# Optimization experiments

Hardware: AMD Instinct MI355X
Metric: run time of the kernel (lower is better)

Reference implementation:

```python
import jax, jax.numpy as jnp
import numpy as np

H = 32          # heads
E = 32          # head dim = mdl_channels // heads (must equal heads per module bug)
C = 1024        # mdl_channels == in_channels
MAXP = 128      # max_position_embeddings
EPS = 1e-5


def _layernorm(x, g, b):
    mu = jnp.mean(x, axis=-1, keepdims=True)
    var = jnp.var(x, axis=-1, keepdims=True)
    return (x - mu) * jax.lax.rsqrt(var + EPS) * g + b


def setup_inputs() -> dict:
    key = jax.random.key(0)
    ks = jax.random.split(key, 16)
    s = 0.02
    N, L = 4, 1024
    inp = {
        "x": jax.random.normal(ks[0], (N, L, C), jnp.float32),
        "Wq": jax.random.normal(ks[1], (C, C), jnp.float32) * s,
        "bq": jnp.zeros((C,), jnp.float32),
        "Wk": jax.random.normal(ks[2], (C, C), jnp.float32) * s,
        "bk": jnp.zeros((C,), jnp.float32),
        "Wv": jax.random.normal(ks[3], (C, C), jnp.float32) * s,
        "bv": jnp.zeros((C,), jnp.float32),
        "dist_emb": jax.random.normal(ks[4], (2 * MAXP + 1, E), jnp.float32) * s,
        "ln1_g": jnp.ones((C,), jnp.float32),
        "ln1_b": jnp.zeros((C,), jnp.float32),
        "ln2_g": jnp.ones((C,), jnp.float32),
        "ln2_b": jnp.zeros((C,), jnp.float32),
        "W1": jax.random.normal(ks[5], (C, C), jnp.float32) * s,
        "b1": jnp.zeros((C,), jnp.float32),
        "W2": jax.random.normal(ks[6], (C, C), jnp.float32) * s,
        "b2": jnp.zeros((C,), jnp.float32),
    }
    return inp


def reference(x, Wq, bq, Wk, bk, Wv, bv, dist_emb, ln1_g, ln1_b,
              ln2_g, ln2_b, W1, b1, W2, b2):
    N, L, _ = x.shape
    # QKV projections -> (N, L, H, E)
    q = (x @ Wq + bq).reshape(N, L, H, E)
    k = (x @ Wk + bk).reshape(N, L, H, E)
    v = (x @ Wv + bv).reshape(N, L, H, E)

    temp = 1.0 / np.sqrt(E).astype(np.float32)
    # content scores (N, H, L, S)
    QK = jnp.einsum('nlhe,nshe->nhls', q, k)
    # relative position scores (disentangled attention)
    pos = jnp.arange(L)
    dist = jnp.clip(pos[:, None] - pos[None, :], -MAXP, MAXP) + MAXP  # (L, L)
    pe = dist_emb[dist]                                              # (L, L, E)
    QK = QK + jnp.einsum('nlhe,lse->nhls', q, pe) \
            + jnp.einsum('nshe,lse->nhls', k, pe)
    A = jax.nn.softmax(temp * QK, axis=-1)          # dropout: eval mode (identity)
    t = jnp.einsum('nhls,nshe->nlhe', A, v).reshape(N, L, C)

    h = _layernorm(t + x, ln1_g, ln1_b)             # AddNorm (attention)
    m = jax.nn.relu(h @ W1 + b1) @ W2 + b2          # 2-layer MLP
    out = _layernorm(m + h, ln2_g, ln2_b)           # AddNorm (mlp)
    return jnp.swapaxes(out, 0, 1)                  # 'n f c -> f n c'
```

## Files before the change

kernel.cpp:

```cpp
#include <hip/hip_runtime.h>

#define H_ 32
#define E_ 32
#define C_ 1024
#define L_ 1024
#define N_ 4
#define M_ 4096
#define NH_ 128
#define D_ 257
#define DPAD 272
#define QDP 264
#define TEMP_ 0.17677669529663687f
#define QSCALE_ (TEMP_ * 1.4426950408889634f)

typedef unsigned short u16;
typedef __attribute__((ext_vector_type(8))) short short8;
typedef __attribute__((ext_vector_type(4))) float f32x4;
typedef __attribute__((ext_vector_type(4))) unsigned short u16x4;

__device__ __forceinline__ u16 f2bf(float f) {
  union { float f; unsigned u; } v; v.f = f;
  unsigned r = v.u + 0x7fffu + ((v.u >> 16) & 1u);
  return (u16)(r >> 16);
}
__device__ __forceinline__ float bf2f(u16 h) {
  union { unsigned u; float f; } v; v.u = ((unsigned)h) << 16;
  return v.f;
}
__device__ __forceinline__ f32x4 mfma16(short8 a, short8 b, f32x4 c) {
  return __builtin_amdgcn_mfma_f32_16x16x32_bf16(a, b, c, 0, 0, 0);
}
__device__ __forceinline__ float ex2(float x) {
#if __has_builtin(__builtin_amdgcn_exp2f)
  return __builtin_amdgcn_exp2f(x);
#else
  float r;
  asm("v_exp_f32 %0, %1\n\ts_nop 1" : "=v"(r) : "v"(x));
  return r;
#endif
}
__device__ __forceinline__ void gld16(const u16* g, u16* l) {
  __builtin_amdgcn_global_load_lds(
      (const __attribute__((address_space(1))) unsigned int*)g,
      (__attribute__((address_space(3))) unsigned int*)l, 16, 0, 0);
}

__global__ __launch_bounds__(256) void misc_kernel(
    const float* __restrict__ x, const float* __restrict__ demb,
    const float* __restrict__ bq, const float* __restrict__ bk,
    const float* __restrict__ bv, u16* __restrict__ xb,
    u16* __restrict__ demb_b, float* __restrict__ bqkv) {
  const int b = blockIdx.x, tid = threadIdx.x;
  if (b < 4096) {
    int i = b * 256 + tid;
    f32x4 v = reinterpret_cast<const f32x4*>(x)[i];
    u16x4 o2;
    o2[0] = f2bf(v[0]); o2[1] = f2bf(v[1]); o2[2] = f2bf(v[2]); o2[3] = f2bf(v[3]);
    reinterpret_cast<u16x4*>(xb)[i] = o2;
  } else {
    int i = (b - 4096) * 256 + tid;
    if (i < DPAD * E_) demb_b[i] = (i < D_ * E_) ? f2bf(demb[i]) : (u16)0;
    if (i < C_) { bqkv[i] = bq[i]; bqkv[C_ + i] = bk[i]; bqkv[2 * C_ + i] = bv[i]; }
  }
}

__global__ __launch_bounds__(256) void transpose_w_kernel(
    const float* __restrict__ Wq, const float* __restrict__ Wk,
    const float* __restrict__ Wv, const float* __restrict__ W1,
    const float* __restrict__ W2, u16* __restrict__ out_base) {
  __shared__ float tile[32][33];
  const int z = blockIdx.z;
  const float* in = (z == 0) ? Wq : (z == 1) ? Wk : (z == 2) ? Wv : (z == 3) ? W1 : W2;
  u16* out = out_base + (size_t)z * C_ * C_;
  int j0 = blockIdx.x * 32, c0 = blockIdx.y * 32;
#pragma unroll
  for (int i = 0; i < 4; ++i) {
    int cy = threadIdx.y + i * 8;
    tile[cy][threadIdx.x] = in[(size_t)(c0 + cy) * C_ + j0 + threadIdx.x];
  }
  __syncthreads();
#pragma unroll
  for (int i = 0; i < 4; ++i) {
    int jy = threadIdx.y + i * 8;
    out[(size_t)(j0 + jy) * C_ + c0 + threadIdx.x] = f2bf(tile[threadIdx.x][jy]);
  }
}

template <int EPI>
__global__ __launch_bounds__(256) void gemm128_kernel(
    const u16* __restrict__ A, const u16* __restrict__ Bt, int K,
    const float* __restrict__ bias,
    u16* __restrict__ out0, u16* __restrict__ out1, u16* __restrict__ out2) {
  __shared__ u16 As[128 * 64];
  __shared__ u16 Bs[128 * 64];
  const int bid = blockIdx.x;
  const int m0 = (bid & 31) << 7;
  const int n0 = (bid >> 5) << 7;
  const int tid = threadIdx.x;
  const int w = tid >> 6, lane = tid & 63, lhi = lane >> 4, llo = lane & 15;
  const int wr = w >> 1, wc = w & 1;
  const int w4 = w << 2;
  const int srow = lane >> 3, scol = (lane & 7) << 3;
  f32x4 acc[4][4] = {};
  for (int k0 = 0; k0 < K; k0 += 64) {
#pragma unroll
    for (int j = 0; j < 4; ++j) {
      const int seg = w4 + j;
      const int row = (seg << 3) + srow;
      gld16(&A[(size_t)(m0 + row) * K + k0 + scol], &As[seg << 9]);
      gld16(&Bt[(size_t)(n0 + row) * K + k0 + scol], &Bs[seg << 9]);
    }
    __syncthreads();
#pragma unroll
    for (int kk = 0; kk < 2; ++kk) {
      const int ko = (kk << 5) + lhi * 8;
      short8 af[4], bf[4];
#pragma unroll
      for (int mi = 0; mi < 4; ++mi)
        af[mi] = *reinterpret_cast<const short8*>(&As[(wr * 64 + mi * 16 + llo) * 64 + ko]);
#pragma unroll
      for (int ni = 0; ni < 4; ++ni)
        bf[ni] = *reinterpret_cast<const short8*>(&Bs[(wc * 64 + ni * 16 + llo) * 64 + ko]);
#pragma unroll
      for (int mi = 0; mi < 4; ++mi)
#pragma unroll
        for (int ni = 0; ni < 4; ++ni)
          acc[mi][ni] = mfma16(af[mi], bf[ni], acc[mi][ni]);
    }
    __syncthreads();
  }
#pragma unroll
  for (int mi = 0; mi < 4; ++mi)
#pragma unroll
    for (int ni = 0; ni < 4; ++ni)
#pragma unroll
      for (int r = 0; r < 4; ++r) {
        int row = m0 + wr * 64 + mi * 16 + lhi * 4 + r;
        int col = n0 + wc * 64 + ni * 16 + llo;
        float v = acc[mi][ni][r] + bias[col];
        if constexpr (EPI == 0) {
          int which = col >> 10, jj = col & 1023, h = jj >> 5, e2 = jj & 31;
          int n = row >> 10, l = row & 1023;
          int nh = (n << 5) | h;
          if (which == 0) v *= QSCALE_;
          u16 bvv = f2bf(v);
          if (which == 0)      out0[((size_t)((nh << 10) | l)) * 32 + e2] = bvv;
          else if (which == 1) out1[((size_t)((nh << 10) | l)) * 32 + e2] = bvv;
          else                 out2[(((size_t)(nh * 32 + e2)) << 10) | l] = bvv;
        } else if constexpr (EPI == 1) {
          out0[(size_t)row * C_ + col] = f2bf(fmaxf(v, 0.f));
        } else {
          out0[(size_t)row * C_ + col] = f2bf(v);
        }
      }
}

__global__ __launch_bounds__(256) void qdkd_kernel(
    const u16* __restrict__ src, const u16* __restrict__ demb,
    u16* __restrict__ dst, u16* __restrict__ aux0, u16* __restrict__ aux256) {
  const int wt = blockIdx.x * 4 + (threadIdx.x >> 6);
  const int lane = threadIdx.x & 63, lhi = lane >> 4, llo = lane & 15;
  const int m0 = wt << 4;
  short8 a = *reinterpret_cast<const short8*>(&src[(size_t)(m0 + llo) * E_ + lhi * 8]);
#pragma unroll
  for (int ct = 0; ct < 17; ++ct) {
    int d = ct * 16 + llo;
    short8 b = {0, 0, 0, 0, 0, 0, 0, 0};
    if (d < D_) b = *reinterpret_cast<const short8*>(&demb[d * E_ + lhi * 8]);
    f32x4 c = {};
    c = mfma16(a, b, c);
    if (d < D_) {
#pragma unroll
      for (int r = 0; r < 4; ++r) {
        u16 val = f2bf(c[r] * QSCALE_);
        dst[(size_t)(m0 + lhi * 4 + r) * D_ + d] = val;
        if (d == 0)   aux0[m0 + lhi * 4 + r] = val;
        if (d == 256) aux256[m0 + lhi * 4 + r] = val;
      }
    }
  }
}

__global__ __launch_bounds__(256, 4) void attn_kernel(
    const u16* __restrict__ qw, const u16* __restrict__ kw,
    const u16* __restrict__ vT, const u16* __restrict__ dembp,
    const u16* __restrict__ KDg, const u16* __restrict__ kd0a,
    const u16* __restrict__ kd256a, u16* __restrict__ tb) {
  __shared__ u16 QDs[64 * QDP];
  __shared__ u16 Pbuf[4 * 512];
  const int bid = blockIdx.x;
  const int nh = bid & (NH_ - 1);
  const int l0 = (bid >> 7) << 6;
  const int tid = threadIdx.x;
  const int w = tid >> 6, lane = tid & 63, lhi = lane >> 4, llo = lane & 15;
  const int lw0 = l0 + (w << 4);
  const int lg = lw0 + llo;
  const int lrow = (w << 4) + llo;

  const u16* qb  = qw + (size_t)nh * (L_ * E_);
  const u16* kb  = kw + (size_t)nh * (L_ * E_);
  const u16* vb  = vT + (size_t)nh * (E_ * L_);
  const u16* kdg = KDg + (size_t)nh * ((size_t)L_ * D_);
  const u16* k0g = kd0a + (size_t)nh * L_;
  const u16* k2g = kd256a + (size_t)nh * L_;

  const short8 qA = *(const short8*)&qb[(size_t)lg * E_ + lhi * 8];
  const int qr4 = (w << 4) + (lhi << 2);

#pragma unroll
  for (int dt = 0; dt < 16; ++dt) {
    short8 db = *(const short8*)&dembp[(dt * 16 + llo) * E_ + lhi * 8];
    f32x4 qd = {};
    qd = mfma16(qA, db, qd);
#pragma unroll
    for (int r = 0; r < 4; ++r)
      QDs[(qr4 + r) * QDP + dt * 16 + llo] = f2bf(qd[r]);
  }
  {
    short8 db = *(const short8*)&dembp[(size_t)(256 + llo) * E_ + lhi * 8];
    f32x4 qd = {};
    qd = mfma16(qA, db, qd);
    if (llo == 0) {
#pragma unroll
      for (int r = 0; r < 4; ++r)
        QDs[(qr4 + r) * QDP + 256] = f2bf(qd[r]);
    }
  }

  const float qd0   = bf2f(QDs[lrow * QDP + 0]);
  const float qd256 = bf2f(QDs[lrow * QDP + 256]);

  f32x4 o0 = {}, o1 = {};
  float lacc = 0.f;
  char* Pw = reinterpret_cast<char*>(&Pbuf[w * 512]);

  for (int s0 = 0; s0 < L_; s0 += 32) {
    short8 kA0 = *(const short8*)&kb[(size_t)(s0 + llo) * E_ + lhi * 8];
    short8 kA1 = *(const short8*)&kb[(size_t)(s0 + 16 + llo) * E_ + lhi * 8];
    f32x4 st0 = {}, st1 = {};
    st0 = mfma16(kA0, qA, st0);
    st1 = mfma16(kA1, qA, st1);

    float p[8];
    const bool far_hi = (lw0 - (s0 + 31)) >= 128;
    const bool far_lo = (s0 - (lw0 + 15)) >= 128;
    if (far_hi || far_lo) {
      const float qdc = far_hi ? qd256 : qd0;
      const u16* kcg = far_hi ? k2g : k0g;
      u16x4 kc0 = *(const u16x4*)&kcg[s0 + lhi * 4];
      u16x4 kc1 = *(const u16x4*)&kcg[s0 + 16 + lhi * 4];
#pragma unroll
      for (int r = 0; r < 4; ++r) {
        p[r]     = ex2(st0[r] + qdc + bf2f(kc0[r]));
        p[4 + r] = ex2(st1[r] + qdc + bf2f(kc1[r]));
      }
    } else {
#pragma unroll
      for (int i = 0; i < 2; ++i)
#pragma unroll
        for (int r = 0; r < 4; ++r) {
          const int scol = s0 + i * 16 + lhi * 4 + r;
          int d = lg - scol;
          d = (d < -128 ? -128 : (d > 128 ? 128 : d)) + 128;
          float qd = bf2f(QDs[lrow * QDP + d]);
          float kd = bf2f(kdg[(size_t)scol * D_ + d]);
          p[i * 4 + r] = ex2((i ? st1[r] : st0[r]) + qd + kd);
        }
    }
    lacc += ((p[0] + p[1]) + (p[2] + p[3])) + ((p[4] + p[5]) + (p[6] + p[7]));

#pragma unroll
    for (int i = 0; i < 2; ++i)
#pragma unroll
      for (int b = 0; b < 2; ++b) {
        union { float f; unsigned u; } a0, a1;
        a0.f = p[i * 4 + 2 * b]; a1.f = p[i * 4 + 2 * b + 1];
        unsigned wv = ((a0.u + 0x8000u) >> 16) | ((a1.u + 0x8000u) & 0xffff0000u);
        int u = (i * 4 + lhi) ^ (llo & 6);
        *reinterpret_cast<unsigned*>(Pw + llo * 64 + u * 8 + b * 4) = wv;
      }
    short8 pB = *reinterpret_cast<const short8*>(
        Pw + llo * 64 + (((lhi * 2) ^ (llo & 6)) * 8));
    short8 vA0 = *(const short8*)&vb[(size_t)llo * L_ + s0 + lhi * 8];
    short8 vA1 = *(const short8*)&vb[(size_t)(16 + llo) * L_ + s0 + lhi * 8];
    o0 = mfma16(vA0, pB, o0);
    o1 = mfma16(vA1, pB, o1);
  }

  float l2 = lacc + __shfl_xor(lacc, 16);
  float lt = l2 + __shfl_xor(l2, 32);
  const float inv = 1.0f / lt;

  const int n = nh >> 5, h = nh & 31;
  const size_t obase = (((size_t)((n << 10) | lg)) * 32 + h) * 32;
  u16x4 w0, w1;
#pragma unroll
  for (int r = 0; r < 4; ++r) {
    w0[r] = f2bf(o0[r] * inv);
    w1[r] = f2bf(o1[r] * inv);
  }
  *reinterpret_cast<u16x4*>(&tb[obase + lhi * 4]) = w0;
  *reinterpret_cast<u16x4*>(&tb[obase + 16 + lhi * 4]) = w1;
}

__global__ __launch_bounds__(256) void ln1_kernel(
    const u16* __restrict__ tbuf, const float* __restrict__ x,
    const float* __restrict__ g, const float* __restrict__ b,
    u16* __restrict__ hb) {
  __shared__ float red[8];
  const int row = blockIdx.x, tid = threadIdx.x;
  const size_t base = (size_t)row * C_ + tid * 4;
  f32x4 xv = *reinterpret_cast<const f32x4*>(&x[base]);
  u16x4 tv = *reinterpret_cast<const u16x4*>(&tbuf[base]);
  float v[4]; float s1 = 0.f, s2 = 0.f;
#pragma unroll
  for (int i = 0; i < 4; ++i) {
    v[i] = xv[i] + bf2f(tv[i]);
    s1 += v[i]; s2 += v[i] * v[i];
  }
#pragma unroll
  for (int off = 32; off >= 1; off >>= 1) {
    s1 += __shfl_xor(s1, off); s2 += __shfl_xor(s2, off);
  }
  if ((tid & 63) == 0) { red[tid >> 6] = s1; red[4 + (tid >> 6)] = s2; }
  __syncthreads();
  float S1 = red[0] + red[1] + red[2] + red[3];
  float S2 = red[4] + red[5] + red[6] + red[7];
  float mu = S1 * (1.f / C_);
  float rs = rsqrtf(S2 * (1.f / C_) - mu * mu + 1e-5f);
#pragma unroll
  for (int i = 0; i < 4; ++i) {
    int c = tid * 4 + i;
    hb[base + i] = f2bf((v[i] - mu) * rs * g[c] + b[c]);
  }
}

__global__ __launch_bounds__(256) void ln2_kernel(
    const u16* __restrict__ mb, const u16* __restrict__ hb,
    const float* __restrict__ g, const float* __restrict__ b,
    float* __restrict__ out) {
  __shared__ float red[8];
  const int row = blockIdx.x, tid = threadIdx.x;
  const size_t base = (size_t)row * C_ + tid * 4;
  u16x4 mv = *reinterpret_cast<const u16x4*>(&mb[base]);
  u16x4 hv = *reinterpret_cast<const u16x4*>(&hb[base]);
  float v[4]; float s1 = 0.f, s2 = 0.f;
#pragma unroll
  for (int i = 0; i < 4; ++i) {
    v[i] = bf2f(mv[i]) + bf2f(hv[i]);
    s1 += v[i]; s2 += v[i] * v[i];
  }
#pragma unroll
  for (int off = 32; off >= 1; off >>= 1) {
    s1 += __shfl_xor(s1, off); s2 += __shfl_xor(s2, off);
  }
  if ((tid & 63) == 0) { red[tid >> 6] = s1; red[4 + (tid >> 6)] = s2; }
  __syncthreads();
  float S1 = red[0] + red[1] + red[2] + red[3];
  float S2 = red[4] + red[5] + red[6] + red[7];
  float mu = S1 * (1.f / C_);
  float rs = rsqrtf(S2 * (1.f / C_) - mu * mu + 1e-5f);
  const int n = row >> 10, l = row & 1023;
  const size_t ob = (size_t)(l * N_ + n) * C_ + tid * 4;
#pragma unroll
  for (int i = 0; i < 4; ++i) {
    int c = tid * 4 + i;
    out[ob + i] = (v[i] - mu) * rs * g[c] + b[c];
  }
}

extern "C" void kernel_launch(void* const* d_in, const int* in_sizes, int n_in,
                              void* d_out, int out_size, void* d_ws, size_t ws_size,
                              hipStream_t stream) {
  const float* x    = (const float*)d_in[0];
  const float* Wq   = (const float*)d_in[1];
  const float* bq   = (const float*)d_in[2];
  const float* Wk   = (const float*)d_in[3];
  const float* bk   = (const float*)d_in[4];
  const float* Wv   = (const float*)d_in[5];
  const float* bv   = (const float*)d_in[6];
  const float* demb = (const float*)d_in[7];
  const float* g1   = (const float*)d_in[8];
  const float* b1ln = (const float*)d_in[9];
  const float* g2   = (const float*)d_in[10];
  const float* b2ln = (const float*)d_in[11];
  const float* W1   = (const float*)d_in[12];
  const float* b1   = (const float*)d_in[13];
  const float* W2   = (const float*)d_in[14];
  const float* b2   = (const float*)d_in[15];
  float* outp = (float*)d_out;

  size_t o = 0;
  auto alloc = [&](size_t bytes) { size_t r = o; o += (bytes + 255) & ~(size_t)255; return r; };
  const size_t xb_o    = alloc((size_t)M_ * C_ * 2);
  const size_t wqkv_o  = alloc((size_t)3 * C_ * C_ * 2);
  const size_t w1_o    = alloc((size_t)C_ * C_ * 2);
  const size_t w2_o    = alloc((size_t)C_ * C_ * 2);
  const size_t bqkv_o  = alloc((size_t)3 * C_ * 4);
  const size_t demb_o  = alloc((size_t)DPAD * E_ * 2);
  const size_t q_o     = alloc((size_t)NH_ * L_ * E_ * 2);
  const size_t k_o     = alloc((size_t)NH_ * L_ * E_ * 2);
  const size_t vt_o    = alloc((size_t)NH_ * L_ * E_ * 2);
  const size_t kd_o    = alloc((size_t)NH_ * L_ * D_ * 2);
  const size_t kd0_o   = alloc((size_t)NH_ * L_ * 2);
  const size_t kd256_o = alloc((size_t)NH_ * L_ * 2);
  const size_t t_o     = alloc((size_t)M_ * C_ * 2);
  const size_t h_o     = alloc((size_t)M_ * C_ * 2);
  const size_t m1_o    = alloc((size_t)M_ * C_ * 2);
  const size_t m_o     = alloc((size_t)M_ * C_ * 2);
  if (o > ws_size) return;

  char* ws = (char*)d_ws;
  u16*   xb     = (u16*)(ws + xb_o);
  u16*   wqkv_t = (u16*)(ws + wqkv_o);
  u16*   w1_t   = (u16*)(ws + w1_o);
  u16*   w2_t   = (u16*)(ws + w2_o);
  float* bqkv   = (float*)(ws + bqkv_o);
  u16*   demb_b = (u16*)(ws + demb_o);
  u16*   q_ws   = (u16*)(ws + q_o);
  u16*   k_ws   = (u16*)(ws + k_o);
  u16*   vT_ws  = (u16*)(ws + vt_o);
  u16*   KD     = (u16*)(ws + kd_o);
  u16*   kd0a   = (u16*)(ws + kd0_o);
  u16*   kd256a = (u16*)(ws + kd256_o);
  u16*   t_b16  = (u16*)(ws + t_o);
  u16*   h_b16  = (u16*)(ws + h_o);
  u16*   m1_b16 = (u16*)(ws + m1_o);
  u16*   m_b16  = (u16*)(ws + m_o);

  misc_kernel<<<4096 + 34, 256, 0, stream>>>(x, demb, bq, bk, bv, xb, demb_b, bqkv);
  dim3 tb_(32, 8), tg_(32, 32, 5);
  transpose_w_kernel<<<tg_, tb_, 0, stream>>>(Wq, Wk, Wv, W1, W2, wqkv_t);

  gemm128_kernel<0><<<32 * 24, 256, 0, stream>>>(xb, wqkv_t, C_, bqkv, q_ws, k_ws, vT_ws);

  qdkd_kernel<<<2048, 256, 0, stream>>>(k_ws, demb_b, KD, kd0a, kd256a);

  attn_kernel<<<NH_ * 16, 256, 0, stream>>>(q_ws, k_ws, vT_ws, demb_b, KD, kd0a, kd256a, t_b16);

  ln1_kernel<<<M_, 256, 0, stream>>>(t_b16, x, g1, b1ln, h_b16);

  gemm128_kernel<1><<<32 * 8, 256, 0, stream>>>(h_b16, w1_t, C_, b1, m1_b16, nullptr, nullptr);
  gemm128_kernel<2><<<32 * 8, 256, 0, stream>>>(m1_b16, w2_t, C_, b2, m_b16, nullptr, nullptr);

  ln2_kernel<<<M_, 256, 0, stream>>>(m_b16, h_b16, g2, b2ln, outp);
}
```

Baseline: 270.0 us.

## Software-pipeline P·V MFMA across iterations with double-buffered P tile in LDS

Double-buffers the per-wave P tile in LDS so each iteration's P·V MFMA runs one step behind the score computation, overlapping its LDS read and V loads with the next QK MFMA and exp work. V loads move to the top of the iteration. The QD row stride is shrunk from 264 to 256, and the d=256 column is stashed in a register through a small LDS scratch, which keeps total LDS about the same. This adds a branch in the near-diagonal path and changes the LDS bank mapping of QD rows, which may create bank conflicts.

After: 269.5 us. Within noise of the previous version (-0.2%).

```diff
diff --git a/kernel.cpp b/kernel.cpp
--- a/kernel.cpp
+++ b/kernel.cpp
@@ -9,7 +9,7 @@
 #define NH_ 128
 #define D_ 257
 #define DPAD 272
-#define QDP 264
+#define QDS 256
 #define TEMP_ 0.17677669529663687f
 #define QSCALE_ (TEMP_ * 1.4426950408889634f)
 
@@ -186,8 +186,8 @@
     const u16* __restrict__ vT, const u16* __restrict__ dembp,
     const u16* __restrict__ KDg, const u16* __restrict__ kd0a,
     const u16* __restrict__ kd256a, u16* __restrict__ tb) {
-  __shared__ u16 QDs[64 * QDP];
-  __shared__ u16 Pbuf[4 * 512];
+  __shared__ u16 QDs[64 * QDS];
+  __shared__ u16 Pbuf[4 * 1024];
   const int bid = blockIdx.x;
   const int nh = bid & (NH_ - 1);
   const int l0 = (bid >> 7) << 6;
@@ -207,6 +207,8 @@
   const short8 qA = *(const short8*)&qb[(size_t)lg * E_ + lhi * 8];
   const int qr4 = (w << 4) + (lhi << 2);
 
+  char* Pw = reinterpret_cast<char*>(&Pbuf[w * 1024]);
+
 #pragma unroll
   for (int dt = 0; dt < 16; ++dt) {
     short8 db = *(const short8*)&dembp[(dt * 16 + llo) * E_ + lhi * 8];
@@ -214,32 +216,42 @@
     qd = mfma16(qA, db, qd);
 #pragma unroll
     for (int r = 0; r < 4; ++r)
-      QDs[(qr4 + r) * QDP + dt * 16 + llo] = f2bf(qd[r]);
-  }
+      QDs[(qr4 + r) * QDS + dt * 16 + llo] = f2bf(qd[r]);
+  }
+  float qd256;
   {
     short8 db = *(const short8*)&dembp[(size_t)(256 + llo) * E_ + lhi * 8];
     f32x4 qd = {};
     qd = mfma16(qA, db, qd);
+    u16* stash = reinterpret_cast<u16*>(Pw);
     if (llo == 0) {
 #pragma unroll
-      for (int r = 0; r < 4; ++r)
-        QDs[(qr4 + r) * QDP + 256] = f2bf(qd[r]);
-    }
-  }
-
-  const float qd0   = bf2f(QDs[lrow * QDP + 0]);
-  const float qd256 = bf2f(QDs[lrow * QDP + 256]);
+      for (int r = 0; r < 4; ++r) stash[(lhi << 2) + r] = f2bf(qd[r]);
+    }
+    qd256 = bf2f(stash[llo]);
+  }
+  const float qd0 = bf2f(QDs[lrow * QDS + 0]);
 
   f32x4 o0 = {}, o1 = {};
   float lacc = 0.f;
-  char* Pw = reinterpret_cast<char*>(&Pbuf[w * 512]);
+  short8 vp0, vp1;
 
   for (int s0 = 0; s0 < L_; s0 += 32) {
+    const int buf = (s0 >> 5) & 1;
     short8 kA0 = *(const short8*)&kb[(size_t)(s0 + llo) * E_ + lhi * 8];
     short8 kA1 = *(const short8*)&kb[(size_t)(s0 + 16 + llo) * E_ + lhi * 8];
+    short8 vc0 = *(const short8*)&vb[(size_t)llo * L_ + s0 + lhi * 8];
+    short8 vc1 = *(const short8*)&vb[(size_t)(16 + llo) * L_ + s0 + lhi * 8];
     f32x4 st0 = {}, st1 = {};
     st0 = mfma16(kA0, qA, st0);
     st1 = mfma16(kA1, qA, st1);
+
+    if (s0) {
+      short8 pB = *reinterpret_cast<const short8*>(
+          Pw + (buf ^ 1) * 1024 + llo * 64 + (((lhi * 2) ^ (llo & 6)) * 8));
+      o0 = mfma16(vp0, pB, o0);
+      o1 = mfma16(vp1, pB, o1);
+    }
 
     float p[8];
     const bool far_hi = (lw0 - (s0 + 31)) >= 128;
@@ -262,7 +274,8 @@
           const int scol = s0 + i * 16 + lhi * 4 + r;
           int d = lg - scol;
           d = (d < -128 ? -128 : (d > 128 ? 128 : d)) + 128;
-          float qd = bf2f(QDs[lrow * QDP + d]);
+          int dc = d > 255 ? 255 : d;
+          float qd = (d == 256) ? qd256 : bf2f(QDs[lrow * QDS + dc]);
           float kd = bf2f(kdg[(size_t)scol * D_ + d]);
           p[i * 4 + r] = ex2((i ? st1[r] : st0[r]) + qd + kd);
         }
@@ -277,14 +290,16 @@
         a0.f = p[i * 4 + 2 * b]; a1.f = p[i * 4 + 2 * b + 1];
         unsigned wv = ((a0.u + 0x8000u) >> 16) | ((a1.u + 0x8000u) & 0xffff0000u);
         int u = (i * 4 + lhi) ^ (llo & 6);
-        *reinterpret_cast<unsigned*>(Pw + llo * 64 + u * 8 + b * 4) = wv;
+        *reinterpret_cast<unsigned*>(Pw + buf * 1024 + llo * 64 + u * 8 + b * 4) = wv;
       }
+    vp0 = vc0; vp1 = vc1;
+  }
+
+  {
     short8 pB = *reinterpret_cast<const short8*>(
-        Pw + llo * 64 + (((lhi * 2) ^ (llo & 6)) * 8));
-    short8 vA0 = *(const short8*)&vb[(size_t)llo * L_ + s0 + lhi * 8];
-    short8 vA1 = *(const short8*)&vb[(size_t)(16 + llo) * L_ + s0 + lhi * 8];
-    o0 = mfma16(vA0, pB, o0);
-    o1 = mfma16(vA1, pB, o1);
+        Pw + 1024 + llo * 64 + (((lhi * 2) ^ (llo & 6)) * 8));
+    o0 = mfma16(vp0, pB, o0);
+    o1 = mfma16(vp1, pB, o1);
   }
 
   float l2 = lacc + __shfl_xor(lacc, 16);
```

## Store key-distance scores in diagonal band layout and reverse query-distance table

Applied to the files above, without the earlier changes.

The K·dist_emb table is rewritten into a band layout indexed by query row, so that in the attention kernel each lane reads contiguous 4-element vectors instead of strided scalar gathers with per-element clamping. The query-distance shared table is stored reversed with a 257 stride so interior tiles also load contiguous vectors. A three-way split separates far tiles, fully interior tiles (vector loads) and boundary tiles (select between band and clamped endpoint values). This adds branching and relies on correct band index arithmetic. The 257 stride may also introduce misaligned vector reads from shared memory.

Result: slower. 324.1 us (+20.0%).

```diff
diff --git a/kernel.cpp b/kernel.cpp
--- a/kernel.cpp
+++ b/kernel.cpp
@@ -9,7 +9,6 @@
 #define NH_ 128
 #define D_ 257
 #define DPAD 272
-#define QDP 264
 #define TEMP_ 0.17677669529663687f
 #define QSCALE_ (TEMP_ * 1.4426950408889634f)
 
@@ -156,26 +155,30 @@
 }
 
 __global__ __launch_bounds__(256) void qdkd_kernel(
-    const u16* __restrict__ src, const u16* __restrict__ demb,
-    u16* __restrict__ dst, u16* __restrict__ aux0, u16* __restrict__ aux256) {
+    const u16* __restrict__ src, const u16* __restrict__ dembp,
+    u16* __restrict__ kdb, u16* __restrict__ aux0, u16* __restrict__ aux256) {
   const int wt = blockIdx.x * 4 + (threadIdx.x >> 6);
   const int lane = threadIdx.x & 63, lhi = lane >> 4, llo = lane & 15;
   const int m0 = wt << 4;
+  const int head = m0 >> 10;
+  u16* kdbh = kdb + (size_t)head * ((size_t)L_ * D_);
   short8 a = *reinterpret_cast<const short8*>(&src[(size_t)(m0 + llo) * E_ + lhi * 8]);
 #pragma unroll
   for (int ct = 0; ct < 17; ++ct) {
     int d = ct * 16 + llo;
-    short8 b = {0, 0, 0, 0, 0, 0, 0, 0};
-    if (d < D_) b = *reinterpret_cast<const short8*>(&demb[d * E_ + lhi * 8]);
+    short8 b = *reinterpret_cast<const short8*>(&dembp[d * E_ + lhi * 8]);
     f32x4 c = {};
     c = mfma16(a, b, c);
     if (d < D_) {
 #pragma unroll
       for (int r = 0; r < 4; ++r) {
         u16 val = f2bf(c[r] * QSCALE_);
-        dst[(size_t)(m0 + lhi * 4 + r) * D_ + d] = val;
-        if (d == 0)   aux0[m0 + lhi * 4 + r] = val;
-        if (d == 256) aux256[m0 + lhi * 4 + r] = val;
+        const int mrow = m0 + (lhi << 2) + r;
+        const int sl = mrow & 1023;
+        const int lp = sl + d - 128;
+        if (lp >= 0 && lp < L_) kdbh[256 * lp + sl + 128] = val;
+        if (d == 0)   aux0[mrow] = val;
+        if (d == 256) aux256[mrow] = val;
       }
     }
   }
@@ -184,9 +187,9 @@
 __global__ __launch_bounds__(256, 4) void attn_kernel(
     const u16* __restrict__ qw, const u16* __restrict__ kw,
     const u16* __restrict__ vT, const u16* __restrict__ dembp,
-    const u16* __restrict__ KDg, const u16* __restrict__ kd0a,
+    const u16* __restrict__ kdb, const u16* __restrict__ kd0a,
     const u16* __restrict__ kd256a, u16* __restrict__ tb) {
-  __shared__ u16 QDs[64 * QDP];
+  __shared__ u16 QDs[64 * 257];
   __shared__ u16 Pbuf[4 * 512];
   const int bid = blockIdx.x;
   const int nh = bid & (NH_ - 1);
@@ -200,7 +203,7 @@
   const u16* qb  = qw + (size_t)nh * (L_ * E_);
   const u16* kb  = kw + (size_t)nh * (L_ * E_);
   const u16* vb  = vT + (size_t)nh * (E_ * L_);
-  const u16* kdg = KDg + (size_t)nh * ((size_t)L_ * D_);
+  const u16* kdl = kdb + (size_t)nh * ((size_t)L_ * D_) + 256 * (size_t)lg + 128;
   const u16* k0g = kd0a + (size_t)nh * L_;
   const u16* k2g = kd256a + (size_t)nh * L_;
 
@@ -214,7 +217,7 @@
     qd = mfma16(qA, db, qd);
 #pragma unroll
     for (int r = 0; r < 4; ++r)
-      QDs[(qr4 + r) * QDP + dt * 16 + llo] = f2bf(qd[r]);
+      QDs[(qr4 + r) * 257 + 256 - (dt * 16 + llo)] = f2bf(qd[r]);
   }
   {
     short8 db = *(const short8*)&dembp[(size_t)(256 + llo) * E_ + lhi * 8];
@@ -222,13 +225,13 @@
     qd = mfma16(qA, db, qd);
     if (llo == 0) {
 #pragma unroll
-      for (int r = 0; r < 4; ++r)
-        QDs[(qr4 + r) * QDP + 256] = f2bf(qd[r]);
+      for (int r = 0; r < 4; ++r) QDs[(qr4 + r) * 257 + 0] = f2bf(qd[r]);
     }
   }
-
-  const float qd0   = bf2f(QDs[lrow * QDP + 0]);
-  const float qd256 = bf2f(QDs[lrow * QDP + 256]);
+  const int qrb = lrow * 257;
+  const int qpb = qrb + 128 - lg;
+  const float qd_d0   = bf2f(QDs[qrb + 256]);
+  const float qd_d256 = bf2f(QDs[qrb + 0]);
 
   f32x4 o0 = {}, o1 = {};
   float lacc = 0.f;
@@ -242,11 +245,11 @@
     st1 = mfma16(kA1, qA, st1);
 
     float p[8];
-    const bool far_hi = (lw0 - (s0 + 31)) >= 128;
-    const bool far_lo = (s0 - (lw0 + 15)) >= 128;
-    if (far_hi || far_lo) {
-      const float qdc = far_hi ? qd256 : qd0;
-      const u16* kcg = far_hi ? k2g : k0g;
+    const int delta = lw0 - s0;
+    if (delta >= 159 || delta <= -143) {
+      const bool fh = delta >= 159;
+      const float qdc = fh ? qd_d256 : qd_d0;
+      const u16* kcg = fh ? k2g : k0g;
       u16x4 kc0 = *(const u16x4*)&kcg[s0 + lhi * 4];
       u16x4 kc1 = *(const u16x4*)&kcg[s0 + 16 + lhi * 4];
 #pragma unroll
@@ -254,17 +257,36 @@
         p[r]     = ex2(st0[r] + qdc + bf2f(kc0[r]));
         p[4 + r] = ex2(st1[r] + qdc + bf2f(kc1[r]));
       }
+    } else if (delta <= 112 && delta >= -97) {
+      u16x4 qv0 = *(const u16x4*)&QDs[qpb + s0 + (lhi << 2)];
+      u16x4 qv1 = *(const u16x4*)&QDs[qpb + s0 + 16 + (lhi << 2)];
+      u16x4 kv0 = *(const u16x4*)&kdl[s0 + (lhi << 2)];
+      u16x4 kv1 = *(const u16x4*)&kdl[s0 + 16 + (lhi << 2)];
+#pragma unroll
+      for (int r = 0; r < 4; ++r) {
+        p[r]     = ex2(st0[r] + bf2f(qv0[r]) + bf2f(kv0[r]));
+        p[4 + r] = ex2(st1[r] + bf2f(qv1[r]) + bf2f(kv1[r]));
+      }
     } else {
+      u16x4 kv0 = *(const u16x4*)&kdl[s0 + (lhi << 2)];
+      u16x4 kv1 = *(const u16x4*)&kdl[s0 + 16 + (lhi << 2)];
+      u16x4 a00 = *(const u16x4*)&k0g[s0 + (lhi << 2)];
+      u16x4 a01 = *(const u16x4*)&k0g[s0 + 16 + (lhi << 2)];
+      u16x4 a20 = *(const u16x4*)&k2g[s0 + (lhi << 2)];
+      u16x4 a21 = *(const u16x4*)&k2g[s0 + 16 + (lhi << 2)];
 #pragma unroll
       for (int i = 0; i < 2; ++i)
 #pragma unroll
         for (int r = 0; r < 4; ++r) {
-          const int scol = s0 + i * 16 + lhi * 4 + r;
-          int d = lg - scol;
-          d = (d < -128 ? -128 : (d > 128 ? 128 : d)) + 128;
-          float qd = bf2f(QDs[lrow * QDP + d]);
-          float kd = bf2f(kdg[(size_t)scol * D_ + d]);
-          p[i * 4 + r] = ex2((i ? st1[r] : st0[r]) + qd + kd);
+          const int scol = s0 + i * 16 + (lhi << 2) + r;
+          int j = scol - lg + 128;
+          int jc = j < 0 ? 0 : (j > 256 ? 256 : j);
+          float qd = bf2f(QDs[qrb + jc]);
+          u16 kin = i ? kv1[r] : kv0[r];
+          u16 klo = i ? a01[r] : a00[r];
+          u16 khi = i ? a21[r] : a20[r];
+          u16 ksel = (j <= 0) ? khi : ((j >= 256) ? klo : kin);
+          p[i * 4 + r] = ex2((i ? st1[r] : st0[r]) + qd + bf2f(ksel));
         }
     }
     lacc += ((p[0] + p[1]) + (p[2] + p[3])) + ((p[4] + p[5]) + (p[6] + p[7]));
@@ -401,7 +423,7 @@
   const size_t q_o     = alloc((size_t)NH_ * L_ * E_ * 2);
   const size_t k_o     = alloc((size_t)NH_ * L_ * E_ * 2);
   const size_t vt_o    = alloc((size_t)NH_ * L_ * E_ * 2);
-  const size_t kd_o    = alloc((size_t)NH_ * L_ * D_ * 2);
+  const size_t kdb_o   = alloc((size_t)NH_ * L_ * D_ * 2);
   const size_t kd0_o   = alloc((size_t)NH_ * L_ * 2);
   const size_t kd256_o = alloc((size_t)NH_ * L_ * 2);
   const size_t t_o     = alloc((size_t)M_ * C_ * 2);
@@ -420,7 +442,7 @@
   u16*   q_ws   = (u16*)(ws + q_o);
   u16*   k_ws   = (u16*)(ws + k_o);
   u16*   vT_ws  = (u16*)(ws + vt_o);
-  u16*   KD     = (u16*)(ws + kd_o);
+  u16*   kdb    = (u16*)(ws + kdb_o);
   u16*   kd0a   = (u16*)(ws + kd0_o);
   u16*   kd256a = (u16*)(ws + kd256_o);
   u16*   t_b16  = (u16*)(ws + t_o);
@@ -434,9 +456,9 @@
 
   gemm128_kernel<0><<<32 * 24, 256, 0, stream>>>(xb, wqkv_t, C_, bqkv, q_ws, k_ws, vT_ws);
 
-  qdkd_kernel<<<2048, 256, 0, stream>>>(k_ws, demb_b, KD, kd0a, kd256a);
-
-  attn_kernel<<<NH_ * 16, 256, 0, stream>>>(q_ws, k_ws, vT_ws, demb_b, KD, kd0a, kd256a, t_b16);
+  qdkd_kernel<<<2048, 256, 0, stream>>>(k_ws, demb_b, kdb, kd0a, kd256a);
+
+  attn_kernel<<<NH_ * 16, 256, 0, stream>>>(q_ws, k_ws, vT_ws, demb_b, kdb, kd0a, kd256a, t_b16);
 
   ln1_kernel<<<M_, 256, 0, stream>>>(t_b16, x, g1, b1ln, h_b16);
 
```

## Add 64x128 GEMM for MLP layers and shrink attention QD shared buffer

Applied to the files above, without the earlier changes.

Adds a gemm64 kernel with 64-row tiles so the two MLP GEMMs launch 512 blocks instead of 256, aiming to fill more of the GPU's compute units. In the attention kernel the per-row QD table stride drops from 264 to 256. The d==256 entry is now passed through a register via a small stash in the P buffer, which cuts LDS use and may raise occupancy. The qdkd kernel also drops a bounds check on the demb load, so it relies on the padded demb buffer; the new 256-element stride could bring back LDS bank conflicts.

After: 264.7 us. No clear change (-1.9%).

```diff
diff --git a/kernel.cpp b/kernel.cpp
--- a/kernel.cpp
+++ b/kernel.cpp
@@ -9,7 +9,7 @@
 #define NH_ 128
 #define D_ 257
 #define DPAD 272
-#define QDP 264
+#define QDS 256
 #define TEMP_ 0.17677669529663687f
 #define QSCALE_ (TEMP_ * 1.4426950408889634f)
 
@@ -155,6 +155,66 @@
       }
 }
 
+template <int EPI>
+__global__ __launch_bounds__(256, 4) void gemm64_kernel(
+    const u16* __restrict__ A, const u16* __restrict__ Bt, int K,
+    const float* __restrict__ bias, u16* __restrict__ out0) {
+  __shared__ u16 As[64 * 64];
+  __shared__ u16 Bs[128 * 64];
+  const int bid = blockIdx.x;
+  const int m0 = (bid & 63) << 6;
+  const int n0 = (bid >> 6) << 7;
+  const int tid = threadIdx.x;
+  const int w = tid >> 6, lane = tid & 63, lhi = lane >> 4, llo = lane & 15;
+  const int wr = w >> 1, wc = w & 1;
+  const int srow = lane >> 3, scol = (lane & 7) << 3;
+  f32x4 acc[2][4] = {};
+  for (int k0 = 0; k0 < K; k0 += 64) {
+#pragma unroll
+    for (int j = 0; j < 2; ++j) {
+      const int seg = w * 2 + j;
+      const int row = (seg << 3) + srow;
+      gld16(&A[(size_t)(m0 + row) * K + k0 + scol], &As[seg << 9]);
+    }
+#pragma unroll
+    for (int j = 0; j < 4; ++j) {
+      const int seg = w * 4 + j;
+      const int row = (seg << 3) + srow;
+      gld16(&Bt[(size_t)(n0 + row) * K + k0 + scol], &Bs[seg << 9]);
+    }
+    __syncthreads();
+#pragma unroll
+    for (int kk = 0; kk < 2; ++kk) {
+      const int ko = (kk << 5) + lhi * 8;
+      short8 af[2], bf[4];
+#pragma unroll
+      for (int mi = 0; mi < 2; ++mi)
+        af[mi] = *reinterpret_cast<const short8*>(&As[(wr * 32 + mi * 16 + llo) * 64 + ko]);
+#pragma unroll
+      for (int ni = 0; ni < 4; ++ni)
+        bf[ni] = *reinterpret_cast<const short8*>(&Bs[(wc * 64 + ni * 16 + llo) * 64 + ko]);
+#pragma unroll
+      for (int mi = 0; mi < 2; ++mi)
+#pragma unroll
+        for (int ni = 0; ni < 4; ++ni)
+          acc[mi][ni] = mfma16(af[mi], bf[ni], acc[mi][ni]);
+    }
+    __syncthreads();
+  }
+#pragma unroll
+  for (int mi = 0; mi < 2; ++mi)
+#pragma unroll
+    for (int ni = 0; ni < 4; ++ni)
+#pragma unroll
+      for (int r = 0; r < 4; ++r) {
+        int row = m0 + wr * 32 + mi * 16 + lhi * 4 + r;
+        int col = n0 + wc * 64 + ni * 16 + llo;
+        float v = acc[mi][ni][r] + bias[col];
+        if constexpr (EPI == 1) out0[(size_t)row * C_ + col] = f2bf(fmaxf(v, 0.f));
+        else                    out0[(size_t)row * C_ + col] = f2bf(v);
+      }
+}
+
 __global__ __launch_bounds__(256) void qdkd_kernel(
     const u16* __restrict__ src, const u16* __restrict__ demb,
     u16* __restrict__ dst, u16* __restrict__ aux0, u16* __restrict__ aux256) {
@@ -165,8 +225,7 @@
 #pragma unroll
   for (int ct = 0; ct < 17; ++ct) {
     int d = ct * 16 + llo;
-    short8 b = {0, 0, 0, 0, 0, 0, 0, 0};
-    if (d < D_) b = *reinterpret_cast<const short8*>(&demb[d * E_ + lhi * 8]);
+    short8 b = *reinterpret_cast<const short8*>(&demb[d * E_ + lhi * 8]);
     f32x4 c = {};
     c = mfma16(a, b, c);
     if (d < D_) {
@@ -186,7 +245,7 @@
     const u16* __restrict__ vT, const u16* __restrict__ dembp,
     const u16* __restrict__ KDg, const u16* __restrict__ kd0a,
     const u16* __restrict__ kd256a, u16* __restrict__ tb) {
-  __shared__ u16 QDs[64 * QDP];
+  __shared__ u16 QDs[64 * QDS];
   __shared__ u16 Pbuf[4 * 512];
   const int bid = blockIdx.x;
   const int nh = bid & (NH_ - 1);
@@ -207,6 +266,8 @@
   const short8 qA = *(const short8*)&qb[(size_t)lg * E_ + lhi * 8];
   const int qr4 = (w << 4) + (lhi << 2);
 
+  char* Pw = reinterpret_cast<char*>(&Pbuf[w * 512]);
+
 #pragma unroll
   for (int dt = 0; dt < 16; ++dt) {
     short8 db = *(const short8*)&dembp[(dt * 16 + llo) * E_ + lhi * 8];
@@ -214,25 +275,24 @@
     qd = mfma16(qA, db, qd);
 #pragma unroll
     for (int r = 0; r < 4; ++r)
-      QDs[(qr4 + r) * QDP + dt * 16 + llo] = f2bf(qd[r]);
-  }
+      QDs[(qr4 + r) * QDS + dt * 16 + llo] = f2bf(qd[r]);
+  }
+  float qd256;
   {
     short8 db = *(const short8*)&dembp[(size_t)(256 + llo) * E_ + lhi * 8];
     f32x4 qd = {};
     qd = mfma16(qA, db, qd);
+    u16* stash = reinterpret_cast<u16*>(Pw);
     if (llo == 0) {
 #pragma unroll
-      for (int r = 0; r < 4; ++r)
-        QDs[(qr4 + r) * QDP + 256] = f2bf(qd[r]);
-    }
-  }
-
-  const float qd0   = bf2f(QDs[lrow * QDP + 0]);
-  const float qd256 = bf2f(QDs[lrow * QDP + 256]);
+      for (int r = 0; r < 4; ++r) stash[(lhi << 2) + r] = f2bf(qd[r]);
+    }
+    qd256 = bf2f(stash[llo]);
+  }
+  const float qd0 = bf2f(QDs[lrow * QDS + 0]);
 
   f32x4 o0 = {}, o1 = {};
   float lacc = 0.f;
-  char* Pw = reinterpret_cast<char*>(&Pbuf[w * 512]);
 
   for (int s0 = 0; s0 < L_; s0 += 32) {
     short8 kA0 = *(const short8*)&kb[(size_t)(s0 + llo) * E_ + lhi * 8];
@@ -262,7 +322,8 @@
           const int scol = s0 + i * 16 + lhi * 4 + r;
           int d = lg - scol;
           d = (d < -128 ? -128 : (d > 128 ? 128 : d)) + 128;
-          float qd = bf2f(QDs[lrow * QDP + d]);
+          int dc = d > 255 ? 255 : d;
+          float qd = (d == 256) ? qd256 : bf2f(QDs[lrow * QDS + dc]);
           float kd = bf2f(kdg[(size_t)scol * D_ + d]);
           p[i * 4 + r] = ex2((i ? st1[r] : st0[r]) + qd + kd);
         }
@@ -440,8 +501,8 @@
 
   ln1_kernel<<<M_, 256, 0, stream>>>(t_b16, x, g1, b1ln, h_b16);
 
-  gemm128_kernel<1><<<32 * 8, 256, 0, stream>>>(h_b16, w1_t, C_, b1, m1_b16, nullptr, nullptr);
-  gemm128_kernel<2><<<32 * 8, 256, 0, stream>>>(m1_b16, w2_t, C_, b2, m_b16, nullptr, nullptr);
+  gemm64_kernel<1><<<64 * 8, 256, 0, stream>>>(h_b16, w1_t, C_, b1, m1_b16);
+  gemm64_kernel<2><<<64 * 8, 256, 0, stream>>>(m1_b16, w2_t, C_, b2, m_b16);
 
   ln2_kernel<<<M_, 256, 0, stream>>>(m_b16, h_b16, g2, b2ln, outp);
 }
```
